# Kernel optimization log

Hardware: AMD Instinct MI355X
Metric: run time of the kernel (lower is better)

The kernel has to match this reference:

```python
import jax, jax.numpy as jnp
import numpy as np

MARGIN = 0.2
SCALE = 30.0

def setup_inputs() -> dict:
    key = jax.random.key(0)
    k1, k2 = jax.random.split(key)
    B, D, C = 8192, 512, 100
    embeddings = jax.random.normal(k1, (B, D), dtype=jnp.float32)
    labels = jax.random.randint(k2, (B,), 0, C, dtype=jnp.int64)
    return {"embeddings": embeddings, "labels": labels}

def reference(embeddings, labels):
    # Cosine similarity via one GEMM: normalize rows once, then n @ n.T.
    # (torch F.cosine_similarity uses eps=1e-8 on norms)
    norms = jnp.maximum(jnp.linalg.norm(embeddings, axis=1, keepdims=True), 1e-8)
    n = embeddings / norms                      # [B, D]
    sim = n @ n.T                               # [B, B]
    pos_mask = labels[:, None] == labels[None, :]  # includes diagonal, as in original
    e = jnp.exp(SCALE * (sim - MARGIN))         # [B, B]
    pos_sum = jnp.sum(jnp.where(pos_mask, e, 0.0))
    neg_sum = jnp.sum(jnp.where(pos_mask, 0.0, e))
    loss = jnp.log1p(neg_sum / pos_sum)
    return loss
```

## Files before the change

kernel.cpp:

```cpp
#include <hip/hip_runtime.h>
#include <hip/hip_bf16.h>
#include <math.h>


#define BDIM 8192
#define DDIM 512
#define MARGIN 0.2f
#define SCALE 30.0f

#define BM 128
#define BN 128
#define BK 32
#define NKT (DDIM / BK)
#define NTILES (BDIM / BM)
#define NBLK (NTILES * (NTILES + 1) / 2)

typedef __hip_bfloat16 bf16;
using f32x4  = __attribute__((ext_vector_type(4))) float;
using bf16x8 = __attribute__((ext_vector_type(8))) short;
using us8    = __attribute__((ext_vector_type(8))) unsigned short;

#define GLOAD_LDS16(gp, lp)                                                    \
    __builtin_amdgcn_global_load_lds(                                          \
        (const __attribute__((address_space(1))) unsigned int*)(gp),           \
        (__attribute__((address_space(3))) unsigned int*)(lp), 16, 0, 0)

__device__ __forceinline__ unsigned short f2bf(float x) {
    union { bf16 h; unsigned short u; } c;
    c.h = __float2bfloat16(x);
    return c.u;
}

__global__ __launch_bounds__(256)
void norm_rows_kernel(const float* __restrict__ emb, bf16* __restrict__ nout) {
    const int row  = blockIdx.x * 4 + (threadIdx.x >> 6);
    const int lane = threadIdx.x & 63;
    const float4* src = (const float4*)(emb + (size_t)row * DDIM) + lane * 2;
    const float4 a = src[0];
    const float4 b = src[1];
    float ss = a.x * a.x + a.y * a.y + a.z * a.z + a.w * a.w
             + b.x * b.x + b.y * b.y + b.z * b.z + b.w * b.w;
    #pragma unroll
    for (int off = 1; off < 64; off <<= 1) ss += __shfl_xor(ss, off, 64);
    const float inv = 1.0f / fmaxf(sqrtf(ss), 1e-8f);

    float v[8] = { a.x, a.y, a.z, a.w, b.x, b.y, b.z, b.w };
    us8 o;
    #pragma unroll
    for (int i = 0; i < 8; ++i) o[i] = f2bf(v[i] * inv);
    *((us8*)(nout + (size_t)row * DDIM) + lane) = o;
}

__global__ __launch_bounds__(256, 4)
void gemm_loss_kernel(const bf16* __restrict__ nmat,
                      const int* __restrict__ labels,
                      double* __restrict__ accum ) {
    const int l = blockIdx.x;
    auto off = [](int b) { return (129 * b - b * b) >> 1; };
    int bi = (int)((129.0 - sqrt(16641.0 - 8.0 * (double)l)) * 0.5);
    if (bi < 0) bi = 0;
    if (bi > 63) bi = 63;
    while (bi > 0 && off(bi) > l) --bi;
    while (off(bi + 1) <= l) ++bi;
    const int bj = bi + (l - off(bi));

    __shared__ alignas(16) short As[2][BM * BK];
    __shared__ alignas(16) short Bs[2][BN * BK];
    __shared__ int    lr[BM];
    __shared__ int    lc[BN];
    __shared__ double red[8];

    const int t = threadIdx.x;
    const int wave = t >> 6;
    const int lane = t & 63;

    if (t < 128) lr[t] = labels[bi * BM + t];
    else         lc[t - 128] = labels[bj * BN + (t - 128)];

    const int wr = wave >> 1;
    const int wc = wave & 1;

    f32x4 acc[4][4] = {};

    const int srow = (lane >> 2);
    const int scol = (lane & 3) * 8;
    const bf16* gA0 = nmat + (size_t)(bi * BM + wave * 16 + srow) * DDIM + scol;
    const bf16* gA1 = gA0 + (size_t)64 * DDIM;
    const bf16* gB0 = nmat + (size_t)(bj * BN + wave * 16 + srow) * DDIM + scol;
    const bf16* gB1 = gB0 + (size_t)64 * DDIM;

    const int frow = lane & 15;
    const int koff = (lane >> 4) * 8;

    auto STAGE = [&](int buf, int kt) {
        const int k0 = kt * BK;
        GLOAD_LDS16(gA0 + k0, &As[buf][(wave * 16) * BK]);
        GLOAD_LDS16(gA1 + k0, &As[buf][(64 + wave * 16) * BK]);
        GLOAD_LDS16(gB0 + k0, &Bs[buf][(wave * 16) * BK]);
        GLOAD_LDS16(gB1 + k0, &Bs[buf][(64 + wave * 16) * BK]);
    };
    auto COMPUTE = [&](int buf) {
        bf16x8 af[4], bfr[4];
        #pragma unroll
        for (int m = 0; m < 4; ++m)
            af[m] = *(const bf16x8*)&As[buf][(wr * 64 + m * 16 + frow) * BK + koff];
        #pragma unroll
        for (int n = 0; n < 4; ++n)
            bfr[n] = *(const bf16x8*)&Bs[buf][(wc * 64 + n * 16 + frow) * BK + koff];
        #pragma unroll
        for (int m = 0; m < 4; ++m)
            #pragma unroll
            for (int n = 0; n < 4; ++n)
                acc[m][n] = __builtin_amdgcn_mfma_f32_16x16x32_bf16(
                    af[m], bfr[n], acc[m][n], 0, 0, 0);
    };

    STAGE(0, 0);
    STAGE(1, 1);
    #pragma unroll 2
    for (int kt = 0; kt < NKT - 2; ++kt) {
        asm volatile("s_waitcnt vmcnt(4)" ::: "memory");
        __builtin_amdgcn_s_barrier();
        asm volatile("" ::: "memory");
        COMPUTE(kt & 1);
        asm volatile("" ::: "memory");
        __builtin_amdgcn_s_barrier();
        asm volatile("" ::: "memory");
        STAGE(kt & 1, kt + 2);
    }
    asm volatile("s_waitcnt vmcnt(4)" ::: "memory");
    __builtin_amdgcn_s_barrier();
    asm volatile("" ::: "memory");
    COMPUTE((NKT - 2) & 1);
    asm volatile("s_waitcnt vmcnt(0)" ::: "memory");
    __builtin_amdgcn_s_barrier();
    asm volatile("" ::: "memory");
    COMPUTE((NKT - 1) & 1);

    float posf = 0.0f, negf = 0.0f;
    const int rbase = wr * 64 + (lane >> 4) * 4;
    const int cbase = wc * 64 + (lane & 15);
    #pragma unroll
    for (int m = 0; m < 4; ++m) {
        #pragma unroll
        for (int nn = 0; nn < 4; ++nn) {
            const int ljv = lc[cbase + nn * 16];
            #pragma unroll
            for (int r = 0; r < 4; ++r) {
                const float sim = acc[m][nn][r];
                const float e = __expf(fmaf(sim, SCALE, -SCALE * MARGIN));
                if (lr[rbase + m * 16 + r] == ljv) posf += e; else negf += e;
            }
        }
    }

    double dp = (double)posf, dn = (double)negf;
    #pragma unroll
    for (int o = 32; o > 0; o >>= 1) {
        dp += __shfl_down(dp, o, 64);
        dn += __shfl_down(dn, o, 64);
    }
    if (lane == 0) { red[wave * 2] = dp; red[wave * 2 + 1] = dn; }
    __syncthreads();
    if (t == 0) {
        const double w = (bi == bj) ? 1.0 : 2.0;
        double p = (red[0] + red[2]) + (red[4] + red[6]);
        double q = (red[1] + red[3]) + (red[5] + red[7]);
        atomicAdd(&accum[0], p * w);
        atomicAdd(&accum[1], q * w);
    }
}

__global__ void finalize_kernel(const double* __restrict__ accum,
                                float* __restrict__ out) {
    if (threadIdx.x == 0 && blockIdx.x == 0) {
        const double r = accum[1] / accum[0];
        out[0] = (float)log1p(r);
    }
}

extern "C" void kernel_launch(void* const* d_in, const int* in_sizes, int n_in,
                              void* d_out, int out_size, void* d_ws, size_t ws_size,
                              hipStream_t stream) {
    const float* emb   = (const float*)d_in[0];
    const int* labels  = (const int*)d_in[1];
    float* out         = (float*)d_out;

    double* accum = (double*)d_ws;
    bf16* nmat    = (bf16*)((char*)d_ws + 256);

    hipMemsetAsync(d_ws, 0, 256, stream);
    norm_rows_kernel<<<BDIM / 4, 256, 0, stream>>>(emb, nmat);
    gemm_loss_kernel<<<NBLK, 256, 0, stream>>>(nmat, labels, accum);
    finalize_kernel<<<1, 64, 0, stream>>>(accum, out);
}
```

Before: 143.8 us.

## Use 256x256 tiles with swizzled LDS, interleaved staging, and fused finalize

Moves the GEMM from 128x128 to 256x256 tiles with BK=64 and 512-thread blocks, which halves global traffic per output element. LDS chunks are XOR-swizzled to avoid bank conflicts, and the next tile's loads are interleaved between MFMA groups under s_setprio. The memset and the finalize kernel are removed: the norm kernel zeroes the accumulators and a last-block atomic counter computes the final loss. The cost is only 528 blocks on a large GPU and heavier register and LDS use.

```diff
diff --git a/kernel.cpp b/kernel.cpp
--- a/kernel.cpp
+++ b/kernel.cpp
@@ -8,12 +8,11 @@
 #define MARGIN 0.2f
 #define SCALE 30.0f
 
-#define BM 128
-#define BN 128
-#define BK 32
+#define BT 256
+#define BK 64
 #define NKT (DDIM / BK)
-#define NTILES (BDIM / BM)
-#define NBLK (NTILES * (NTILES + 1) / 2)
+#define NT (BDIM / BT)
+#define NBLK (NT * (NT + 1) / 2)
 
 typedef __hip_bfloat16 bf16;
 using f32x4  = __attribute__((ext_vector_type(4))) float;
@@ -32,7 +31,11 @@
 }
 
 __global__ __launch_bounds__(256)
-void norm_rows_kernel(const float* __restrict__ emb, bf16* __restrict__ nout) {
+void norm_rows_kernel(const float* __restrict__ emb, bf16* __restrict__ nout,
+                      double* __restrict__ accum, unsigned* __restrict__ ctr) {
+    if (blockIdx.x == 0 && threadIdx.x == 0) {
+        accum[0] = 0.0; accum[1] = 0.0; *ctr = 0u;
+    }
     const int row  = blockIdx.x * 4 + (threadIdx.x >> 6);
     const int lane = threadIdx.x & 63;
     const float4* src = (const float4*)(emb + (size_t)row * DDIM) + lane * 2;
@@ -43,7 +46,6 @@
     #pragma unroll
     for (int off = 1; off < 64; off <<= 1) ss += __shfl_xor(ss, off, 64);
     const float inv = 1.0f / fmaxf(sqrtf(ss), 1e-8f);
-
     float v[8] = { a.x, a.y, a.z, a.w, b.x, b.y, b.z, b.w };
     us8 o;
     #pragma unroll
@@ -51,104 +53,147 @@
     *((us8*)(nout + (size_t)row * DDIM) + lane) = o;
 }
 
-__global__ __launch_bounds__(256, 4)
+__global__ __launch_bounds__(512, 2)
 void gemm_loss_kernel(const bf16* __restrict__ nmat,
                       const int* __restrict__ labels,
-                      double* __restrict__ accum ) {
+                      double* __restrict__ accum, unsigned* __restrict__ ctr,
+                      float* __restrict__ out) {
     const int l = blockIdx.x;
-    auto off = [](int b) { return (129 * b - b * b) >> 1; };
-    int bi = (int)((129.0 - sqrt(16641.0 - 8.0 * (double)l)) * 0.5);
-    if (bi < 0) bi = 0;
-    if (bi > 63) bi = 63;
-    while (bi > 0 && off(bi) > l) --bi;
-    while (off(bi + 1) <= l) ++bi;
-    const int bj = bi + (l - off(bi));
-
-    __shared__ alignas(16) short As[2][BM * BK];
-    __shared__ alignas(16) short Bs[2][BN * BK];
-    __shared__ int    lr[BM];
-    __shared__ int    lc[BN];
-    __shared__ double red[8];
-
-    const int t = threadIdx.x;
-    const int wave = t >> 6;
-    const int lane = t & 63;
-
-    if (t < 128) lr[t] = labels[bi * BM + t];
-    else         lc[t - 128] = labels[bj * BN + (t - 128)];
-
-    const int wr = wave >> 1;
-    const int wc = wave & 1;
-
-    f32x4 acc[4][4] = {};
-
-    const int srow = (lane >> 2);
-    const int scol = (lane & 3) * 8;
-    const bf16* gA0 = nmat + (size_t)(bi * BM + wave * 16 + srow) * DDIM + scol;
-    const bf16* gA1 = gA0 + (size_t)64 * DDIM;
-    const bf16* gB0 = nmat + (size_t)(bj * BN + wave * 16 + srow) * DDIM + scol;
-    const bf16* gB1 = gB0 + (size_t)64 * DDIM;
-
-    const int frow = lane & 15;
-    const int koff = (lane >> 4) * 8;
-
-    auto STAGE = [&](int buf, int kt) {
-        const int k0 = kt * BK;
-        GLOAD_LDS16(gA0 + k0, &As[buf][(wave * 16) * BK]);
-        GLOAD_LDS16(gA1 + k0, &As[buf][(64 + wave * 16) * BK]);
-        GLOAD_LDS16(gB0 + k0, &Bs[buf][(wave * 16) * BK]);
-        GLOAD_LDS16(gB1 + k0, &Bs[buf][(64 + wave * 16) * BK]);
-    };
-    auto COMPUTE = [&](int buf) {
-        bf16x8 af[4], bfr[4];
-        #pragma unroll
-        for (int m = 0; m < 4; ++m)
-            af[m] = *(const bf16x8*)&As[buf][(wr * 64 + m * 16 + frow) * BK + koff];
-        #pragma unroll
-        for (int n = 0; n < 4; ++n)
-            bfr[n] = *(const bf16x8*)&Bs[buf][(wc * 64 + n * 16 + frow) * BK + koff];
-        #pragma unroll
-        for (int m = 0; m < 4; ++m)
-            #pragma unroll
-            for (int n = 0; n < 4; ++n)
-                acc[m][n] = __builtin_amdgcn_mfma_f32_16x16x32_bf16(
-                    af[m], bfr[n], acc[m][n], 0, 0, 0);
-    };
-
-    STAGE(0, 0);
-    STAGE(1, 1);
+    auto tri = [](int b) { return ((65 - b) * b) >> 1; };
+    int bi = (int)((65.0 - sqrt(4225.0 - 8.0 * (double)l)) * 0.5);
+    bi = bi < 0 ? 0 : (bi > 31 ? 31 : bi);
+    while (bi > 0 && tri(bi) > l) --bi;
+    while (tri(bi + 1) <= l) ++bi;
+    const int bj = bi + (l - tri(bi));
+
+    __shared__ short As[2][BT * BK];
+    __shared__ short Bs[2][BT * BK];
+    __shared__ int lr[BT], lc[BT];
+    __shared__ double red[16];
+
+    const int t = threadIdx.x, wid = t >> 6, lane = t & 63;
+    if (t < 256) lr[t] = labels[bi * BT + t];
+    else         lc[t - 256] = labels[bj * BT + (t - 256)];
+
+    const int wm = wid >> 2;
+    const int wn = wid & 3;
+
+    const int srow = wid * 16 + (lane >> 3);
+    const int swz8 = ((lane & 7) ^ (lane >> 3)) * 8;
+    const bf16* gA = nmat + (size_t)(bi * BT + srow) * DDIM + swz8;
+    const bf16* gB = nmat + (size_t)(bj * BT + srow) * DDIM + swz8;
+    const int ldsw = wid * 1024;
+
+    #define STAGE_A(buf, kt, h)                                                 \
+        do {                                                                    \
+            GLOAD_LDS16(gA + (size_t)(h) * 128 * DDIM + (kt) * BK,              \
+                        &As[buf][(h) * 8192 + ldsw]);                           \
+            GLOAD_LDS16(gA + (size_t)(h) * 128 * DDIM + 8 * DDIM + (kt) * BK,   \
+                        &As[buf][(h) * 8192 + ldsw + 512]);                     \
+        } while (0)
+    #define STAGE_B(buf, kt, h)                                                 \
+        do {                                                                    \
+            GLOAD_LDS16(gB + (size_t)(h) * 128 * DDIM + (kt) * BK,              \
+                        &Bs[buf][(h) * 8192 + ldsw]);                           \
+            GLOAD_LDS16(gB + (size_t)(h) * 128 * DDIM + 8 * DDIM + (kt) * BK,   \
+                        &Bs[buf][(h) * 8192 + ldsw + 512]);                     \
+        } while (0)
+
+    const int arow = (wm * 128 + (lane & 15)) * BK;
+    const int brow = (wn * 64 + (lane & 15)) * BK;
+    const int chk0 = (((lane >> 4) + 0) ^ (lane & 7)) * 8;
+    const int chk1 = (((lane >> 4) + 4) ^ (lane & 7)) * 8;
+
+    f32x4 acc[8][4] = {};
+
+    STAGE_A(0, 0, 0); STAGE_A(0, 0, 1); STAGE_B(0, 0, 0); STAGE_B(0, 0, 1);
+
     #pragma unroll 2
-    for (int kt = 0; kt < NKT - 2; ++kt) {
-        asm volatile("s_waitcnt vmcnt(4)" ::: "memory");
+    for (int kt = 0; kt < NKT; ++kt) {
+        const int cur = kt & 1, nxt = cur ^ 1;
+        const bool more = (kt + 1 < NKT);
+        if (more) {
+            STAGE_A(nxt, kt + 1, 0);
+            asm volatile("s_waitcnt vmcnt(2)" ::: "memory");
+        } else {
+            asm volatile("s_waitcnt vmcnt(0)" ::: "memory");
+        }
         __builtin_amdgcn_s_barrier();
         asm volatile("" ::: "memory");
-        COMPUTE(kt & 1);
-        asm volatile("" ::: "memory");
+
+        bf16x8 a[4], b[4], a2[4];
+        #pragma unroll
+        for (int m = 0; m < 4; ++m)
+            a[m] = *(const bf16x8*)&As[cur][arow + m * 1024 + chk0];
+        #pragma unroll
+        for (int n = 0; n < 4; ++n)
+            b[n] = *(const bf16x8*)&Bs[cur][brow + n * 1024 + chk0];
+        if (more) STAGE_A(nxt, kt + 1, 1);
+        __builtin_amdgcn_s_setprio(1);
+        #pragma unroll
+        for (int m = 0; m < 4; ++m)
+            #pragma unroll
+            for (int n = 0; n < 4; ++n)
+                acc[m][n] = __builtin_amdgcn_mfma_f32_16x16x32_bf16(
+                    a[m], b[n], acc[m][n], 0, 0, 0);
+        __builtin_amdgcn_s_setprio(0);
+        #pragma unroll
+        for (int m = 0; m < 4; ++m)
+            a2[m] = *(const bf16x8*)&As[cur][arow + (m + 4) * 1024 + chk0];
+        if (more) STAGE_B(nxt, kt + 1, 0);
+        __builtin_amdgcn_s_setprio(1);
+        #pragma unroll
+        for (int m = 0; m < 4; ++m)
+            #pragma unroll
+            for (int n = 0; n < 4; ++n)
+                acc[m + 4][n] = __builtin_amdgcn_mfma_f32_16x16x32_bf16(
+                    a2[m], b[n], acc[m + 4][n], 0, 0, 0);
+        __builtin_amdgcn_s_setprio(0);
+        #pragma unroll
+        for (int m = 0; m < 4; ++m)
+            a[m] = *(const bf16x8*)&As[cur][arow + m * 1024 + chk1];
+        #pragma unroll
+        for (int n = 0; n < 4; ++n)
+            b[n] = *(const bf16x8*)&Bs[cur][brow + n * 1024 + chk1];
+        if (more) STAGE_B(nxt, kt + 1, 1);
+        __builtin_amdgcn_s_setprio(1);
+        #pragma unroll
+        for (int m = 0; m < 4; ++m)
+            #pragma unroll
+            for (int n = 0; n < 4; ++n)
+                acc[m][n] = __builtin_amdgcn_mfma_f32_16x16x32_bf16(
+                    a[m], b[n], acc[m][n], 0, 0, 0);
+        __builtin_amdgcn_s_setprio(0);
+        #pragma unroll
+        for (int m = 0; m < 4; ++m)
+            a2[m] = *(const bf16x8*)&As[cur][arow + (m + 4) * 1024 + chk1];
+        asm volatile("s_waitcnt lgkmcnt(0)" ::: "memory");
+        __builtin_amdgcn_sched_barrier(0);
         __builtin_amdgcn_s_barrier();
         asm volatile("" ::: "memory");
-        STAGE(kt & 1, kt + 2);
-    }
-    asm volatile("s_waitcnt vmcnt(4)" ::: "memory");
-    __builtin_amdgcn_s_barrier();
-    asm volatile("" ::: "memory");
-    COMPUTE((NKT - 2) & 1);
-    asm volatile("s_waitcnt vmcnt(0)" ::: "memory");
-    __builtin_amdgcn_s_barrier();
-    asm volatile("" ::: "memory");
-    COMPUTE((NKT - 1) & 1);
+        __builtin_amdgcn_s_setprio(1);
+        #pragma unroll
+        for (int m = 0; m < 4; ++m)
+            #pragma unroll
+            for (int n = 0; n < 4; ++n)
+                acc[m + 4][n] = __builtin_amdgcn_mfma_f32_16x16x32_bf16(
+                    a2[m], b[n], acc[m + 4][n], 0, 0, 0);
+        __builtin_amdgcn_s_setprio(0);
+    }
+    #undef STAGE_A
+    #undef STAGE_B
 
     float posf = 0.0f, negf = 0.0f;
-    const int rbase = wr * 64 + (lane >> 4) * 4;
-    const int cbase = wc * 64 + (lane & 15);
-    #pragma unroll
-    for (int m = 0; m < 4; ++m) {
-        #pragma unroll
-        for (int nn = 0; nn < 4; ++nn) {
-            const int ljv = lc[cbase + nn * 16];
+    const int rbase = wm * 128 + (lane >> 4) * 4;
+    const int cbase = wn * 64 + (lane & 15);
+    #pragma unroll
+    for (int m = 0; m < 8; ++m) {
+        #pragma unroll
+        for (int n = 0; n < 4; ++n) {
+            const int ljv = lc[cbase + n * 16];
             #pragma unroll
             for (int r = 0; r < 4; ++r) {
-                const float sim = acc[m][nn][r];
-                const float e = __expf(fmaf(sim, SCALE, -SCALE * MARGIN));
+                const float e = __expf(fmaf(acc[m][n][r], SCALE, -SCALE * MARGIN));
                 if (lr[rbase + m * 16 + r] == ljv) posf += e; else negf += e;
             }
         }
@@ -160,37 +205,37 @@
         dp += __shfl_down(dp, o, 64);
         dn += __shfl_down(dn, o, 64);
     }
-    if (lane == 0) { red[wave * 2] = dp; red[wave * 2 + 1] = dn; }
+    if (lane == 0) { red[wid * 2] = dp; red[wid * 2 + 1] = dn; }
     __syncthreads();
     if (t == 0) {
         const double w = (bi == bj) ? 1.0 : 2.0;
-        double p = (red[0] + red[2]) + (red[4] + red[6]);
-        double q = (red[1] + red[3]) + (red[5] + red[7]);
+        double p = 0.0, q = 0.0;
+        #pragma unroll
+        for (int i = 0; i < 8; ++i) { p += red[2 * i]; q += red[2 * i + 1]; }
         atomicAdd(&accum[0], p * w);
         atomicAdd(&accum[1], q * w);
-    }
-}
-
-__global__ void finalize_kernel(const double* __restrict__ accum,
-                                float* __restrict__ out) {
-    if (threadIdx.x == 0 && blockIdx.x == 0) {
-        const double r = accum[1] / accum[0];
-        out[0] = (float)log1p(r);
+        __threadfence();
+        unsigned prev = atomicAdd(ctr, 1u);
+        if (prev == NBLK - 1) {
+            __threadfence();
+            double pp = atomicAdd(&accum[0], 0.0);
+            double qq = atomicAdd(&accum[1], 0.0);
+            out[0] = (float)log1p(qq / pp);
+        }
     }
 }
 
 extern "C" void kernel_launch(void* const* d_in, const int* in_sizes, int n_in,
                               void* d_out, int out_size, void* d_ws, size_t ws_size,
                               hipStream_t stream) {
-    const float* emb   = (const float*)d_in[0];
-    const int* labels  = (const int*)d_in[1];
-    float* out         = (float*)d_out;
+    const float* emb  = (const float*)d_in[0];
+    const int* labels = (const int*)d_in[1];
+    float* out        = (float*)d_out;
 
     double* accum = (double*)d_ws;
+    unsigned* ctr = (unsigned*)((char*)d_ws + 16);
     bf16* nmat    = (bf16*)((char*)d_ws + 256);
 
-    hipMemsetAsync(d_ws, 0, 256, stream);
-    norm_rows_kernel<<<BDIM / 4, 256, 0, stream>>>(emb, nmat);
-    gemm_loss_kernel<<<NBLK, 256, 0, stream>>>(nmat, labels, accum);
-    finalize_kernel<<<1, 64, 0, stream>>>(accum, out);
-}
+    norm_rows_kernel<<<BDIM / 4, 256, 0, stream>>>(emb, nmat, accum, ctr);
+    gemm_loss_kernel<<<NBLK, 512, 0, stream>>>(nmat, labels, accum, ctr, out);
+}
```

After: 134.5 us. 6.5% less time.
